# Performance work log

Hardware: AMD Instinct MI355X
Metric: run time of the kernel (lower is better)

Reference implementation:

```python
import jax, jax.numpy as jnp
import numpy as np

N, E, D_IN, H, C = 100000, 1600000, 128, 64, 4
EPS = 1e-5


def _ln(v):
    m = jnp.mean(v, axis=-1, keepdims=True)
    var = jnp.var(v, axis=-1, keepdims=True)
    return (v - m) * jax.lax.rsqrt(var + EPS)


def setup_inputs() -> dict:
    key = jax.random.key(0)
    ks = jax.random.split(key, 16)
    g = lambda k, shp, sc: (jax.random.normal(k, shp, jnp.float32) * sc)
    return {
        "x": g(ks[0], (N, D_IN), 1.0),
        "edge_attr": jax.random.uniform(ks[1], (E, 1), jnp.float32),
        "edge_index": jax.random.randint(ks[2], (2, E), 0, N, dtype=jnp.int32),
        # edge_proj Linear(1,1): keep weights positive so edge weights stay positive
        "We": jnp.full((1, 1), 0.8, jnp.float32),
        "be": jnp.full((1,), 0.2, jnp.float32),
        "W_in": g(ks[3], (D_IN, H), (1.0 / np.sqrt(D_IN))),
        "b_in": jnp.zeros((H,), jnp.float32),
        "W_g": g(ks[4], (3, H, H), (1.0 / np.sqrt(H))),  # 3 GCN layer weights
        "b_g": jnp.zeros((3, H), jnp.float32),
        "Wa1": g(ks[5], (H, H // 2), (1.0 / np.sqrt(H))),
        "ba1": jnp.zeros((H // 2,), jnp.float32),
        "Wa2": g(ks[6], (H // 2, 1), (1.0 / np.sqrt(H // 2))),
        "ba2": jnp.zeros((1,), jnp.float32),
        "Wc1": g(ks[7], (H, H // 2), (1.0 / np.sqrt(H))),
        "bc1": jnp.zeros((H // 2,), jnp.float32),
        "Wc2": g(ks[8], (H // 2, C), (1.0 / np.sqrt(H // 2))),
        "bc2": jnp.zeros((C,), jnp.float32),
    }


def reference(x, edge_attr, edge_index, We, be, W_in, b_in, W_g, b_g,
              Wa1, ba1, Wa2, ba2, Wc1, bc1, Wc2, bc2):
    src, dst = edge_index[0], edge_index[1]
    n = x.shape[0]
    # input projection
    h = jax.nn.relu(x @ W_in + b_in)
    # edge weights from edge_proj(edge_attr)
    ew = (edge_attr @ We + be)[:, 0]  # [E]
    # GCN symmetric norm with self-loops (loop weight 1.0), as in PyG GCNConv
    deg = jax.ops.segment_sum(ew, dst, num_segments=n) + 1.0
    dinv = jnp.where(deg > 0, jax.lax.rsqrt(deg), 0.0)
    norm = dinv[src] * ew * dinv[dst]      # [E]
    self_norm = dinv * dinv                # [N]
    for i in range(3):
        residual = h
        hw = h @ W_g[i]                                            # [N,H]
        agg = jax.ops.segment_sum(hw[src] * norm[:, None], dst,
                                  num_segments=n)                  # gather-scale-scatter
        out = agg + hw * self_norm[:, None] + b_g[i]
        out = jax.nn.relu(_ln(out))  # layer_norm path (batch is None); dropout = eval identity
        if i > 0:
            out = out + residual
        h = out
    attn = jax.nn.sigmoid(jax.nn.relu(h @ Wa1 + ba1) @ Wa2 + ba2)  # [N,1]
    h = h * attn
    logits = jax.nn.relu(h @ Wc1 + bc1) @ Wc2 + bc2                # [N,C]
    return logits, attn
```

## Files before the change

kernel.cpp:

```cpp
#include <hip/hip_runtime.h>
#include <hip/hip_bf16.h>

#define HID 64
#define DIN 128
#define NCLS 4

__device__ __forceinline__ float bcast(float v, int l) {
    return __uint_as_float(__builtin_amdgcn_readlane(__float_as_uint(v), l));
}
__device__ __forceinline__ ushort f2bf(float f) {
    unsigned u = __float_as_uint(f);
    return (ushort)((u + 0x7fffu + ((u >> 16) & 1u)) >> 16);
}
__device__ __forceinline__ float bflo(unsigned v) { return __uint_as_float(v << 16); }
__device__ __forceinline__ float bfhi(unsigned v) { return __uint_as_float(v & 0xffff0000u); }


__global__ __launch_bounds__(256) void degrank_kernel(const float* __restrict__ ea,
                                                      const int* __restrict__ dst,
                                                      const float* __restrict__ We,
                                                      const float* __restrict__ be,
                                                      unsigned long long* __restrict__ pk,
                                                      int* __restrict__ rank, int E) {
    int e = blockIdx.x * blockDim.x + threadIdx.x;
    if (e >= E) return;
    float ew = ea[e] * We[0] + be[0];
    unsigned long long fx = (unsigned long long)(ew * 1048576.0f + 0.5f);
    unsigned long long old = atomicAdd(&pk[dst[e]], (1ull << 40) | fx);
    rank[e] = (int)(old >> 40);
}

__global__ __launch_bounds__(256) void unpack_scan1_kernel(const unsigned long long* __restrict__ pk,
                                                           float* __restrict__ dinv,
                                                           int* __restrict__ scanned,
                                                           int* __restrict__ bsum, int N) {
    int t = blockIdx.x * 256 + threadIdx.x;
    int lane = threadIdx.x & 63, w = threadIdx.x >> 6;
    int cnt = 0;
    if (t < N) {
        unsigned long long v = pk[t];
        cnt = (int)(v >> 40);
        float deg = (float)((double)(v & ((1ull << 40) - 1)) * (1.0 / 1048576.0));
        dinv[t] = rsqrtf(deg + 1.0f);
    }
    int xv = cnt;
#pragma unroll
    for (int off = 1; off < 64; off <<= 1) {
        int y = __shfl_up(xv, off);
        if (lane >= off) xv += y;
    }
    __shared__ int ws_[4];
    if (lane == 63) ws_[w] = xv;
    __syncthreads();
    for (int i = 0; i < w; ++i) xv += ws_[i];
    if (t < N) scanned[t] = xv;
    if (threadIdx.x == 255) bsum[blockIdx.x] = xv;
}

__global__ __launch_bounds__(1024) void scan2_kernel(int* __restrict__ bsum, int nb) {
    int t = threadIdx.x, lane = t & 63, w = t >> 6;
    int x = (t < nb) ? bsum[t] : 0;
#pragma unroll
    for (int off = 1; off < 64; off <<= 1) {
        int y = __shfl_up(x, off);
        if (lane >= off) x += y;
    }
    __shared__ int s16[16];
    if (lane == 63) s16[w] = x;
    __syncthreads();
    if (w == 0) {
        int y = (lane < 16) ? s16[lane] : 0;
#pragma unroll
        for (int off = 1; off < 16; off <<= 1) {
            int z = __shfl_up(y, off);
            if (lane >= off) y += z;
        }
        if (lane < 16) s16[lane] = y;
    }
    __syncthreads();
    if (w > 0) x += s16[w - 1];
    if (t < nb) bsum[t] = x;
}

__global__ __launch_bounds__(256) void scan3_kernel(const int* __restrict__ scanned,
                                                    const int* __restrict__ bsum,
                                                    int* __restrict__ rowptr, int N) {
    int t = blockIdx.x * 256 + threadIdx.x;
    if (t >= N) return;
    int add = (blockIdx.x > 0) ? bsum[blockIdx.x - 1] : 0;
    rowptr[t + 1] = scanned[t] + add;
    if (t == 0) rowptr[0] = 0;
}

__global__ __launch_bounds__(256) void fill_kernel(const float* __restrict__ ea,
                                                   const int* __restrict__ src,
                                                   const int* __restrict__ dst,
                                                   const int* __restrict__ rank,
                                                   const float* __restrict__ We,
                                                   const float* __restrict__ be,
                                                   const int* __restrict__ rowptr,
                                                   float2* __restrict__ srcnorm, int E) {
    int e = blockIdx.x * blockDim.x + threadIdx.x;
    if (e >= E) return;
    float ew = ea[e] * We[0] + be[0];
    int d = dst[e];
    srcnorm[rowptr[d] + rank[e]] = make_float2(__int_as_float(src[e]), ew);
}


__global__ __launch_bounds__(256) void inproj_kernel(const float* __restrict__ x,
                                                     const float* __restrict__ W,
                                                     const float* __restrict__ b,
                                                     const float* __restrict__ dinv,
                                                     float* __restrict__ h,
                                                     unsigned* __restrict__ hs, int N) {
    int lane = threadIdx.x & 63;
    int gw = (blockIdx.x * 256 + threadIdx.x) >> 6;
    int n0 = gw * 4;
    if (n0 >= N) return;
    const float* xr[4];
    float acc[4], dnv[4];
    float bc = b[lane];
#pragma unroll
    for (int j = 0; j < 4; ++j) {
        int n = n0 + j; if (n >= N) n = N - 1;
        xr[j] = x + (long)__builtin_amdgcn_readfirstlane(n) * DIN;
        acc[j] = bc;
        dnv[j] = dinv[n];
    }
#pragma unroll 16
    for (int k = 0; k < DIN; ++k) {
        float wv = W[k * HID + lane];
#pragma unroll
        for (int j = 0; j < 4; ++j)
            acc[j] = fmaf(xr[j][k], wv, acc[j]);
    }
#pragma unroll
    for (int j = 0; j < 4; ++j) {
        int n = n0 + j;
        if (n < N) {
            float hv = fmaxf(acc[j], 0.0f);
            h[((long)n << 6) | lane] = hv;
            unsigned bv = f2bf(hv * dnv[j]);
            unsigned nb = __shfl_xor(bv, 1);
            if ((lane & 1) == 0)
                hs[(unsigned)n * 32 + (lane >> 1)] = bv | (nb << 16);
        }
    }
}


__global__ __launch_bounds__(256) void gather_kernel(const int* __restrict__ rowptr,
                                                     const float2* __restrict__ srcnorm,
                                                     const unsigned* __restrict__ hs,
                                                     const float* __restrict__ dinv,
                                                     float* __restrict__ s, int N) {
    int t = blockIdx.x * blockDim.x + threadIdx.x;
    int lane = t & 63;
    int c2 = lane & 31, hf = lane >> 5;
    int n = __builtin_amdgcn_readfirstlane(t >> 6);
    if (n >= N) return;
    unsigned sv = hs[(unsigned)n * 32 + c2];
    float ax = hf ? 0.0f : bflo(sv);
    float ay = hf ? 0.0f : bfhi(sv);
    int beg = rowptr[n], end = rowptr[n + 1];
    int i = beg;
    int end16 = beg + ((end - beg) & ~15);
    for (; i < end16; i += 16) {
        float2 p0 = srcnorm[i + hf],      p1 = srcnorm[i + 2 + hf];
        float2 p2 = srcnorm[i + 4 + hf],  p3 = srcnorm[i + 6 + hf];
        float2 p4 = srcnorm[i + 8 + hf],  p5 = srcnorm[i + 10 + hf];
        float2 p6 = srcnorm[i + 12 + hf], p7 = srcnorm[i + 14 + hf];
        unsigned v0 = hs[(unsigned)__float_as_int(p0.x) * 32 + c2];
        unsigned v1 = hs[(unsigned)__float_as_int(p1.x) * 32 + c2];
        unsigned v2 = hs[(unsigned)__float_as_int(p2.x) * 32 + c2];
        unsigned v3 = hs[(unsigned)__float_as_int(p3.x) * 32 + c2];
        unsigned v4 = hs[(unsigned)__float_as_int(p4.x) * 32 + c2];
        unsigned v5 = hs[(unsigned)__float_as_int(p5.x) * 32 + c2];
        unsigned v6 = hs[(unsigned)__float_as_int(p6.x) * 32 + c2];
        unsigned v7 = hs[(unsigned)__float_as_int(p7.x) * 32 + c2];
        ax = fmaf(bflo(v0), p0.y, ax); ay = fmaf(bfhi(v0), p0.y, ay);
        ax = fmaf(bflo(v1), p1.y, ax); ay = fmaf(bfhi(v1), p1.y, ay);
        ax = fmaf(bflo(v2), p2.y, ax); ay = fmaf(bfhi(v2), p2.y, ay);
        ax = fmaf(bflo(v3), p3.y, ax); ay = fmaf(bfhi(v3), p3.y, ay);
        ax = fmaf(bflo(v4), p4.y, ax); ay = fmaf(bfhi(v4), p4.y, ay);
        ax = fmaf(bflo(v5), p5.y, ax); ay = fmaf(bfhi(v5), p5.y, ay);
        ax = fmaf(bflo(v6), p6.y, ax); ay = fmaf(bfhi(v6), p6.y, ay);
        ax = fmaf(bflo(v7), p7.y, ax); ay = fmaf(bfhi(v7), p7.y, ay);
    }
    int end8 = i + ((end - i) & ~7);
    for (; i < end8; i += 8) {
        float2 pa = srcnorm[i + hf],     pb = srcnorm[i + 2 + hf];
        float2 pc = srcnorm[i + 4 + hf], pd = srcnorm[i + 6 + hf];
        unsigned va = hs[(unsigned)__float_as_int(pa.x) * 32 + c2];
        unsigned vb = hs[(unsigned)__float_as_int(pb.x) * 32 + c2];
        unsigned vc = hs[(unsigned)__float_as_int(pc.x) * 32 + c2];
        unsigned vd = hs[(unsigned)__float_as_int(pd.x) * 32 + c2];
        ax = fmaf(bflo(va), pa.y, ax); ay = fmaf(bfhi(va), pa.y, ay);
        ax = fmaf(bflo(vb), pb.y, ax); ay = fmaf(bfhi(vb), pb.y, ay);
        ax = fmaf(bflo(vc), pc.y, ax); ay = fmaf(bfhi(vc), pc.y, ay);
        ax = fmaf(bflo(vd), pd.y, ax); ay = fmaf(bfhi(vd), pd.y, ay);
    }
    for (; i < end; i += 2) {
        int ia = i + hf;
        if (ia < end) {
            float2 p = srcnorm[ia];
            unsigned v = hs[(unsigned)__float_as_int(p.x) * 32 + c2];
            ax = fmaf(bflo(v), p.y, ax);
            ay = fmaf(bfhi(v), p.y, ay);
        }
    }
    ax += __shfl_xor(ax, 32);
    ay += __shfl_xor(ay, 32);
    if (hf == 0) {
        float dn = dinv[n];
        ((float2*)(s + ((long)n << 6)))[c2] = make_float2(ax * dn, ay * dn);
    }
}


__global__ __launch_bounds__(256) void dense_kernel(const float* __restrict__ s,
                                                    const float* __restrict__ Wg,
                                                    const float* __restrict__ bg,
                                                    const float* __restrict__ dinv,
                                                    float* __restrict__ h,
                                                    unsigned* __restrict__ hs,
                                                    int add_res, int N) {
    int lane = threadIdx.x & 63;
    int gw = blockIdx.x * 4 + ((int)threadIdx.x >> 6);
    int nw = gridDim.x * 4;
    int withhs = (hs != nullptr);
    float wcol[64];
#pragma unroll
    for (int k = 0; k < 64; ++k) wcol[k] = Wg[k * HID + lane];
    float bgl = bg[lane];
    for (int n0 = gw * 4; n0 < N; n0 += nw * 4) {
        float sv[4], acc[4], rv[4], dnv[4];
#pragma unroll
        for (int j = 0; j < 4; ++j) {
            int n = n0 + j; if (n >= N) n = N - 1;
            sv[j] = s[((long)n << 6) | lane];
            rv[j] = add_res ? h[((long)n << 6) | lane] : 0.0f;
            dnv[j] = withhs ? dinv[n] : 0.0f;
            acc[j] = bgl;
        }
#pragma unroll
        for (int k = 0; k < 64; ++k) {
#pragma unroll
            for (int j = 0; j < 4; ++j)
                acc[j] = fmaf(bcast(sv[j], k), wcol[k], acc[j]);
        }
        float s1[4], s2[4];
#pragma unroll
        for (int j = 0; j < 4; ++j) { s1[j] = acc[j]; s2[j] = acc[j] * acc[j]; }
#pragma unroll
        for (int off = 32; off; off >>= 1) {
#pragma unroll
            for (int j = 0; j < 4; ++j) {
                s1[j] += __shfl_xor(s1[j], off);
                s2[j] += __shfl_xor(s2[j], off);
            }
        }
#pragma unroll
        for (int j = 0; j < 4; ++j) {
            int n = n0 + j;
            float mean = s1[j] * (1.0f / 64.0f);
            float var  = s2[j] * (1.0f / 64.0f) - mean * mean;
            float o = fmaxf((acc[j] - mean) * rsqrtf(var + 1e-5f), 0.0f) + rv[j];
            if (n < N) {
                h[((long)n << 6) | lane] = o;
                if (withhs) {
                    unsigned bv = f2bf(o * dnv[j]);
                    unsigned nb = __shfl_xor(bv, 1);
                    if ((lane & 1) == 0)
                        hs[(unsigned)n * 32 + (lane >> 1)] = bv | (nb << 16);
                }
            }
        }
    }
}


__global__ __launch_bounds__(256) void head_kernel(const float* __restrict__ h,
                                                   const float* __restrict__ Wa1,
                                                   const float* __restrict__ ba1,
                                                   const float* __restrict__ Wa2,
                                                   const float* __restrict__ ba2,
                                                   const float* __restrict__ Wc1,
                                                   const float* __restrict__ bc1,
                                                   const float* __restrict__ Wc2,
                                                   const float* __restrict__ bc2,
                                                   float* __restrict__ out, int N) {
    __shared__ float hsm[4][HID];
    int lane = threadIdx.x & 63, w = threadIdx.x >> 6;
    int jj = lane & 31, hf = lane >> 5;
    float wa1[32], wc1[32];
#pragma unroll
    for (int k = 0; k < 32; ++k) {
        int kk = hf * 32 + k;
        wa1[k] = Wa1[kk * 32 + jj];
        wc1[k] = Wc1[kk * 32 + jj];
    }
    float wa2v = Wa2[jj], ba1v = ba1[jj], ba2v = ba2[0], bc1v = bc1[jj];
    float wc2v[4], bc2v[4];
#pragma unroll
    for (int c = 0; c < 4; ++c) { wc2v[c] = Wc2[jj * 4 + c]; bc2v[c] = bc2[c]; }
    int gw = blockIdx.x * 4 + w, stride = gridDim.x * 4;
    for (int n = gw; n < N; n += stride) {
        float hv = h[((long)n << 6) | lane];
        hsm[w][lane] = hv;
        float a1p = 0.0f, c1p = 0.0f;
#pragma unroll
        for (int k = 0; k < 32; ++k) {
            float hk = hsm[w][hf * 32 + k];
            a1p = fmaf(hk, wa1[k], a1p);
            c1p = fmaf(hk, wc1[k], c1p);
        }
        a1p += __shfl_xor(a1p, 32);
        c1p += __shfl_xor(c1p, 32);
        float a1 = fmaxf(a1p + ba1v, 0.0f);
        float z = a1 * wa2v;
#pragma unroll
        for (int off = 16; off; off >>= 1) z += __shfl_xor(z, off);
        float attn = 1.0f / (1.0f + expf(-(z + ba2v)));
        float c1 = fmaxf(fmaf(attn, c1p, bc1v), 0.0f);
        float o0 = c1 * wc2v[0], o1 = c1 * wc2v[1], o2 = c1 * wc2v[2], o3 = c1 * wc2v[3];
#pragma unroll
        for (int off = 16; off; off >>= 1) {
            o0 += __shfl_xor(o0, off);
            o1 += __shfl_xor(o1, off);
            o2 += __shfl_xor(o2, off);
            o3 += __shfl_xor(o3, off);
        }
        if (lane == 0) {
            float4 ov = make_float4(o0 + bc2v[0], o1 + bc2v[1], o2 + bc2v[2], o3 + bc2v[3]);
            *(float4*)(out + (long)n * NCLS) = ov;
            out[(long)N * NCLS + n] = attn;
        }
    }
}


extern "C" void kernel_launch(void* const* d_in, const int* in_sizes, int n_in,
                              void* d_out, int out_size, void* d_ws, size_t ws_size,
                              hipStream_t stream) {
    const float* x    = (const float*)d_in[0];
    const float* ea   = (const float*)d_in[1];
    const int*   ei   = (const int*)d_in[2];
    const float* We   = (const float*)d_in[3];
    const float* be   = (const float*)d_in[4];
    const float* W_in = (const float*)d_in[5];
    const float* b_in = (const float*)d_in[6];
    const float* W_g  = (const float*)d_in[7];
    const float* b_g  = (const float*)d_in[8];
    const float* Wa1  = (const float*)d_in[9];
    const float* ba1  = (const float*)d_in[10];
    const float* Wa2  = (const float*)d_in[11];
    const float* ba2  = (const float*)d_in[12];
    const float* Wc1  = (const float*)d_in[13];
    const float* bc1  = (const float*)d_in[14];
    const float* Wc2  = (const float*)d_in[15];
    const float* bc2  = (const float*)d_in[16];
    float* out = (float*)d_out;

    const int N = in_sizes[0] / DIN;
    const int E = in_sizes[1];
    const int* srcI = ei;
    const int* dstI = ei + E;
    const int nblk = (N + 255) / 256;

    unsigned long long* pk = (unsigned long long*)d_ws;
    float*    dinv    = (float*)(pk + N);
    float*    h       = dinv + N;
    float*    s       = h + (long)N * HID;
    unsigned* hs      = (unsigned*)(s + (long)N * HID);
    float2*   srcnorm = (float2*)(hs + (long)N * 32);
    int*      scanned = (int*)(srcnorm + E);
    int*      bsum    = scanned + N;
    int*      rowptr  = bsum + 1024;
    int*      rank    = rowptr + N + 1;

    hipMemsetAsync(pk, 0, N * sizeof(unsigned long long), stream);

    degrank_kernel<<<(E + 255) / 256, 256, 0, stream>>>(ea, dstI, We, be, pk, rank, E);
    unpack_scan1_kernel<<<nblk, 256, 0, stream>>>(pk, dinv, scanned, bsum, N);
    scan2_kernel<<<1, 1024, 0, stream>>>(bsum, nblk);
    scan3_kernel<<<nblk, 256, 0, stream>>>(scanned, bsum, rowptr, N);
    fill_kernel<<<(E + 255) / 256, 256, 0, stream>>>(ea, srcI, dstI, rank, We, be,
                                                     rowptr, srcnorm, E);

    inproj_kernel<<<(N + 15) / 16, 256, 0, stream>>>(x, W_in, b_in, dinv, h, hs, N);

    long nt = (long)N * HID;
    gather_kernel<<<(nt + 255) / 256, 256, 0, stream>>>(rowptr, srcnorm, hs, dinv, s, N);
    dense_kernel<<<1024, 256, 0, stream>>>(s, W_g, b_g, dinv, h, hs, 0, N);
    gather_kernel<<<(nt + 255) / 256, 256, 0, stream>>>(rowptr, srcnorm, hs, dinv, s, N);
    dense_kernel<<<1024, 256, 0, stream>>>(s, W_g + HID * HID, b_g + HID, dinv, h, hs, 1, N);
    gather_kernel<<<(nt + 255) / 256, 256, 0, stream>>>(rowptr, srcnorm, hs, dinv, s, N);
    dense_kernel<<<1024, 256, 0, stream>>>(s, W_g + 2 * HID * HID, b_g + 2 * HID, dinv,
                                           h, (unsigned*)nullptr, 1, N);
    head_kernel<<<1024, 256, 0, stream>>>(h, Wa1, ba1, Wa2, ba2,
                                          Wc1, bc1, Wc2, bc2, out, N);
}
```

Measured before the change: 460.0 us.

## Use bf16 MFMA for input projection and GCN dense layers with bf16 aggregate buffer

The scalar FMA input projection and per-layer dense kernels are replaced with kernels using 16x16x32 bf16 MFMA instructions. Weights are converted to bf16 and transposed into shared memory, and LayerNorm statistics are reduced across the MFMA output layout. The gather kernel now writes its aggregate in packed bf16 instead of fp32, halving that intermediate's traffic. The cost is reduced precision in the input features, aggregates and weights, plus a per-block reload of the weights into shared memory.

```diff
diff --git a/kernel.cpp b/kernel.cpp
--- a/kernel.cpp
+++ b/kernel.cpp
@@ -5,15 +5,23 @@
 #define DIN 128
 #define NCLS 4
 
-__device__ __forceinline__ float bcast(float v, int l) {
-    return __uint_as_float(__builtin_amdgcn_readlane(__float_as_uint(v), l));
-}
+typedef __attribute__((ext_vector_type(8))) __bf16 bf16x8;
+typedef __attribute__((ext_vector_type(4))) float f32x4;
+
 __device__ __forceinline__ ushort f2bf(float f) {
     unsigned u = __float_as_uint(f);
     return (ushort)((u + 0x7fffu + ((u >> 16) & 1u)) >> 16);
 }
 __device__ __forceinline__ float bflo(unsigned v) { return __uint_as_float(v << 16); }
 __device__ __forceinline__ float bfhi(unsigned v) { return __uint_as_float(v & 0xffff0000u); }
+
+__device__ __forceinline__ bf16x8 cvt8(const float4* p) {
+    float4 a = p[0], c = p[1];
+    union { ushort u[8]; bf16x8 v; } r;
+    r.u[0] = f2bf(a.x); r.u[1] = f2bf(a.y); r.u[2] = f2bf(a.z); r.u[3] = f2bf(a.w);
+    r.u[4] = f2bf(c.x); r.u[5] = f2bf(c.y); r.u[6] = f2bf(c.z); r.u[7] = f2bf(c.w);
+    return r.v;
+}
 
 
 __global__ __launch_bounds__(256) void degrank_kernel(const float* __restrict__ ea,
@@ -108,43 +116,53 @@
 }
 
 
-__global__ __launch_bounds__(256) void inproj_kernel(const float* __restrict__ x,
-                                                     const float* __restrict__ W,
-                                                     const float* __restrict__ b,
-                                                     const float* __restrict__ dinv,
-                                                     float* __restrict__ h,
-                                                     unsigned* __restrict__ hs, int N) {
+__global__ __launch_bounds__(256) void inproj_mfma_kernel(const float* __restrict__ x,
+                                                          const float* __restrict__ W,
+                                                          const float* __restrict__ b,
+                                                          const float* __restrict__ dinv,
+                                                          float* __restrict__ h,
+                                                          unsigned* __restrict__ hs, int N) {
+    __shared__ ushort Wt[64][DIN + 8];
+    for (int idx = threadIdx.x; idx < DIN * HID; idx += 256) {
+        int k = idx >> 6, c = idx & 63;
+        Wt[c][k] = f2bf(W[idx]);
+    }
+    __syncthreads();
     int lane = threadIdx.x & 63;
-    int gw = (blockIdx.x * 256 + threadIdx.x) >> 6;
-    int n0 = gw * 4;
+    int l15 = lane & 15, kg = lane >> 4;
+    int wv = blockIdx.x * 4 + ((int)threadIdx.x >> 6);
+    int n0 = wv * 16;
     if (n0 >= N) return;
-    const float* xr[4];
-    float acc[4], dnv[4];
-    float bc = b[lane];
-#pragma unroll
-    for (int j = 0; j < 4; ++j) {
-        int n = n0 + j; if (n >= N) n = N - 1;
-        xr[j] = x + (long)__builtin_amdgcn_readfirstlane(n) * DIN;
-        acc[j] = bc;
-        dnv[j] = dinv[n];
-    }
-#pragma unroll 16
-    for (int k = 0; k < DIN; ++k) {
-        float wv = W[k * HID + lane];
-#pragma unroll
-        for (int j = 0; j < 4; ++j)
-            acc[j] = fmaf(xr[j][k], wv, acc[j]);
-    }
-#pragma unroll
-    for (int j = 0; j < 4; ++j) {
-        int n = n0 + j;
-        if (n < N) {
-            float hv = fmaxf(acc[j], 0.0f);
-            h[((long)n << 6) | lane] = hv;
-            unsigned bv = f2bf(hv * dnv[j]);
+    int ar = n0 + l15; if (ar >= N) ar = N - 1;
+    const float* xr = x + (long)ar * DIN;
+    f32x4 z = {0.0f, 0.0f, 0.0f, 0.0f};
+    f32x4 acc[4] = {z, z, z, z};
+#pragma unroll
+    for (int ks = 0; ks < 4; ++ks) {
+        bf16x8 af = cvt8((const float4*)(xr + ks * 32 + kg * 8));
+#pragma unroll
+        for (int ct = 0; ct < 4; ++ct) {
+            bf16x8 bfr = *(const bf16x8*)&Wt[ct * 16 + l15][ks * 32 + kg * 8];
+            acc[ct] = __builtin_amdgcn_mfma_f32_16x16x32_bf16(af, bfr, acc[ct], 0, 0, 0);
+        }
+    }
+    float bgv[4];
+#pragma unroll
+    for (int ct = 0; ct < 4; ++ct) bgv[ct] = b[ct * 16 + l15];
+#pragma unroll
+    for (int r = 0; r < 4; ++r) {
+        int n = n0 + kg * 4 + r;
+        bool ok = (n < N);
+        float dn = ok ? dinv[n] : 0.0f;
+#pragma unroll
+        for (int ct = 0; ct < 4; ++ct) {
+            int c = ct * 16 + l15;
+            float o = fmaxf(acc[ct][r] + bgv[ct], 0.0f);
+            if (ok) h[((long)n << 6) | c] = o;
+            unsigned bv = f2bf(o * dn);
             unsigned nb = __shfl_xor(bv, 1);
-            if ((lane & 1) == 0)
-                hs[(unsigned)n * 32 + (lane >> 1)] = bv | (nb << 16);
+            if (ok && (l15 & 1) == 0)
+                hs[(unsigned)n * 32 + ct * 8 + (l15 >> 1)] = bv | (nb << 16);
         }
     }
 }
@@ -154,7 +172,7 @@
                                                      const float2* __restrict__ srcnorm,
                                                      const unsigned* __restrict__ hs,
                                                      const float* __restrict__ dinv,
-                                                     float* __restrict__ s, int N) {
+                                                     unsigned* __restrict__ sb, int N) {
     int t = blockIdx.x * blockDim.x + threadIdx.x;
     int lane = t & 63;
     int c2 = lane & 31, hf = lane >> 5;
@@ -214,67 +232,90 @@
     ay += __shfl_xor(ay, 32);
     if (hf == 0) {
         float dn = dinv[n];
-        ((float2*)(s + ((long)n << 6)))[c2] = make_float2(ax * dn, ay * dn);
-    }
-}
-
-
-__global__ __launch_bounds__(256) void dense_kernel(const float* __restrict__ s,
-                                                    const float* __restrict__ Wg,
-                                                    const float* __restrict__ bg,
-                                                    const float* __restrict__ dinv,
-                                                    float* __restrict__ h,
-                                                    unsigned* __restrict__ hs,
-                                                    int add_res, int N) {
+        sb[(unsigned)n * 32 + c2] = (unsigned)f2bf(ax * dn) |
+                                    ((unsigned)f2bf(ay * dn) << 16);
+    }
+}
+
+
+__global__ __launch_bounds__(256) void dense_mfma_kernel(const unsigned* __restrict__ sb,
+                                                         const float* __restrict__ Wg,
+                                                         const float* __restrict__ bg,
+                                                         const float* __restrict__ dinv,
+                                                         float* __restrict__ h,
+                                                         unsigned* __restrict__ hs,
+                                                         int add_res, int N) {
+    __shared__ ushort Wt[64][HID + 8];
+    for (int idx = threadIdx.x; idx < HID * HID; idx += 256) {
+        int k = idx >> 6, c = idx & 63;
+        Wt[c][k] = f2bf(Wg[idx]);
+    }
+    __syncthreads();
     int lane = threadIdx.x & 63;
-    int gw = blockIdx.x * 4 + ((int)threadIdx.x >> 6);
-    int nw = gridDim.x * 4;
+    int l15 = lane & 15, kg = lane >> 4;
+    int wv = blockIdx.x * 4 + ((int)threadIdx.x >> 6);
+    int n0 = wv * 16;
+    if (n0 >= N) return;
+    bf16x8 bfr[2][4];
+#pragma unroll
+    for (int ks = 0; ks < 2; ++ks)
+#pragma unroll
+        for (int ct = 0; ct < 4; ++ct)
+            bfr[ks][ct] = *(const bf16x8*)&Wt[ct * 16 + l15][ks * 32 + kg * 8];
+    int ar = n0 + l15; if (ar >= N) ar = N - 1;
+    const uint4* sr = (const uint4*)(sb + (unsigned)ar * 32);
+    bf16x8 af0 = __builtin_bit_cast(bf16x8, sr[kg]);
+    bf16x8 af1 = __builtin_bit_cast(bf16x8, sr[4 + kg]);
+    f32x4 z = {0.0f, 0.0f, 0.0f, 0.0f};
+    f32x4 acc[4];
+#pragma unroll
+    for (int ct = 0; ct < 4; ++ct) {
+        acc[ct] = __builtin_amdgcn_mfma_f32_16x16x32_bf16(af0, bfr[0][ct], z, 0, 0, 0);
+        acc[ct] = __builtin_amdgcn_mfma_f32_16x16x32_bf16(af1, bfr[1][ct], acc[ct], 0, 0, 0);
+    }
+    float bgv[4];
+#pragma unroll
+    for (int ct = 0; ct < 4; ++ct) bgv[ct] = bg[ct * 16 + l15];
+#pragma unroll
+    for (int ct = 0; ct < 4; ++ct)
+#pragma unroll
+        for (int r = 0; r < 4; ++r) acc[ct][r] += bgv[ct];
+    float s1[4], s2[4];
+#pragma unroll
+    for (int r = 0; r < 4; ++r) {
+        s1[r] = acc[0][r] + acc[1][r] + acc[2][r] + acc[3][r];
+        s2[r] = acc[0][r] * acc[0][r] + acc[1][r] * acc[1][r] +
+                acc[2][r] * acc[2][r] + acc[3][r] * acc[3][r];
+    }
+#pragma unroll
+    for (int off = 1; off < 16; off <<= 1) {
+#pragma unroll
+        for (int r = 0; r < 4; ++r) {
+            s1[r] += __shfl_xor(s1[r], off);
+            s2[r] += __shfl_xor(s2[r], off);
+        }
+    }
     int withhs = (hs != nullptr);
-    float wcol[64];
-#pragma unroll
-    for (int k = 0; k < 64; ++k) wcol[k] = Wg[k * HID + lane];
-    float bgl = bg[lane];
-    for (int n0 = gw * 4; n0 < N; n0 += nw * 4) {
-        float sv[4], acc[4], rv[4], dnv[4];
-#pragma unroll
-        for (int j = 0; j < 4; ++j) {
-            int n = n0 + j; if (n >= N) n = N - 1;
-            sv[j] = s[((long)n << 6) | lane];
-            rv[j] = add_res ? h[((long)n << 6) | lane] : 0.0f;
-            dnv[j] = withhs ? dinv[n] : 0.0f;
-            acc[j] = bgl;
-        }
-#pragma unroll
-        for (int k = 0; k < 64; ++k) {
-#pragma unroll
-            for (int j = 0; j < 4; ++j)
-                acc[j] = fmaf(bcast(sv[j], k), wcol[k], acc[j]);
-        }
-        float s1[4], s2[4];
-#pragma unroll
-        for (int j = 0; j < 4; ++j) { s1[j] = acc[j]; s2[j] = acc[j] * acc[j]; }
-#pragma unroll
-        for (int off = 32; off; off >>= 1) {
-#pragma unroll
-            for (int j = 0; j < 4; ++j) {
-                s1[j] += __shfl_xor(s1[j], off);
-                s2[j] += __shfl_xor(s2[j], off);
-            }
-        }
-#pragma unroll
-        for (int j = 0; j < 4; ++j) {
-            int n = n0 + j;
-            float mean = s1[j] * (1.0f / 64.0f);
-            float var  = s2[j] * (1.0f / 64.0f) - mean * mean;
-            float o = fmaxf((acc[j] - mean) * rsqrtf(var + 1e-5f), 0.0f) + rv[j];
-            if (n < N) {
-                h[((long)n << 6) | lane] = o;
-                if (withhs) {
-                    unsigned bv = f2bf(o * dnv[j]);
-                    unsigned nb = __shfl_xor(bv, 1);
-                    if ((lane & 1) == 0)
-                        hs[(unsigned)n * 32 + (lane >> 1)] = bv | (nb << 16);
-                }
+#pragma unroll
+    for (int r = 0; r < 4; ++r) {
+        int n = n0 + kg * 4 + r;
+        bool ok = (n < N);
+        float mean = s1[r] * (1.0f / 64.0f);
+        float var  = s2[r] * (1.0f / 64.0f) - mean * mean;
+        float rsq  = rsqrtf(var + 1e-5f);
+        float dn = (withhs && ok) ? dinv[n] : 0.0f;
+#pragma unroll
+        for (int ct = 0; ct < 4; ++ct) {
+            int c = ct * 16 + l15;
+            long idx = ((long)n << 6) | c;
+            float o = fmaxf((acc[ct][r] - mean) * rsq, 0.0f);
+            if (add_res && ok) o += h[idx];
+            if (ok) h[idx] = o;
+            if (withhs) {
+                unsigned bv = f2bf(o * dn);
+                unsigned nb = __shfl_xor(bv, 1);
+                if (ok && (l15 & 1) == 0)
+                    hs[(unsigned)n * 32 + ct * 8 + (l15 >> 1)] = bv | (nb << 16);
             }
         }
     }
@@ -368,12 +409,13 @@
     const int* srcI = ei;
     const int* dstI = ei + E;
     const int nblk = (N + 255) / 256;
+    const int mblk = ((N + 15) / 16 + 3) / 4;
 
     unsigned long long* pk = (unsigned long long*)d_ws;
     float*    dinv    = (float*)(pk + N);
     float*    h       = dinv + N;
-    float*    s       = h + (long)N * HID;
-    unsigned* hs      = (unsigned*)(s + (long)N * HID);
+    unsigned* sbuf    = (unsigned*)(h + (long)N * HID);
+    unsigned* hs      = sbuf + (long)N * 32;
     float2*   srcnorm = (float2*)(hs + (long)N * 32);
     int*      scanned = (int*)(srcnorm + E);
     int*      bsum    = scanned + N;
@@ -389,16 +431,17 @@
     fill_kernel<<<(E + 255) / 256, 256, 0, stream>>>(ea, srcI, dstI, rank, We, be,
                                                      rowptr, srcnorm, E);
 
-    inproj_kernel<<<(N + 15) / 16, 256, 0, stream>>>(x, W_in, b_in, dinv, h, hs, N);
+    inproj_mfma_kernel<<<mblk, 256, 0, stream>>>(x, W_in, b_in, dinv, h, hs, N);
 
     long nt = (long)N * HID;
-    gather_kernel<<<(nt + 255) / 256, 256, 0, stream>>>(rowptr, srcnorm, hs, dinv, s, N);
-    dense_kernel<<<1024, 256, 0, stream>>>(s, W_g, b_g, dinv, h, hs, 0, N);
-    gather_kernel<<<(nt + 255) / 256, 256, 0, stream>>>(rowptr, srcnorm, hs, dinv, s, N);
-    dense_kernel<<<1024, 256, 0, stream>>>(s, W_g + HID * HID, b_g + HID, dinv, h, hs, 1, N);
-    gather_kernel<<<(nt + 255) / 256, 256, 0, stream>>>(rowptr, srcnorm, hs, dinv, s, N);
-    dense_kernel<<<1024, 256, 0, stream>>>(s, W_g + 2 * HID * HID, b_g + 2 * HID, dinv,
-                                           h, (unsigned*)nullptr, 1, N);
+    gather_kernel<<<(nt + 255) / 256, 256, 0, stream>>>(rowptr, srcnorm, hs, dinv, sbuf, N);
+    dense_mfma_kernel<<<mblk, 256, 0, stream>>>(sbuf, W_g, b_g, dinv, h, hs, 0, N);
+    gather_kernel<<<(nt + 255) / 256, 256, 0, stream>>>(rowptr, srcnorm, hs, dinv, sbuf, N);
+    dense_mfma_kernel<<<mblk, 256, 0, stream>>>(sbuf, W_g + HID * HID, b_g + HID, dinv,
+                                                h, hs, 1, N);
+    gather_kernel<<<(nt + 255) / 256, 256, 0, stream>>>(rowptr, srcnorm, hs, dinv, sbuf, N);
+    dense_mfma_kernel<<<mblk, 256, 0, stream>>>(sbuf, W_g + 2 * HID * HID, b_g + 2 * HID,
+                                                dinv, h, (unsigned*)nullptr, 1, N);
     head_kernel<<<1024, 256, 0, stream>>>(h, Wa1, ba1, Wa2, ba2,
                                           Wc1, bc1, Wc2, bc2, out, N);
 }
```

New measurement: 374.8 us (median of 2 runs). -18.5%, faster.
